# Optimization experiments

Measured on AMD Instinct MI355X. Metric: run time of the kernel, lower is better.

The kernel has to match this reference:

```python
import jax, jax.numpy as jnp
import numpy as np

B, CIN, H = 8192, 512, 2048  # batch, in_channels, hidden_channels


def _ln(x, g, b, eps=1e-5):
    m = jnp.mean(x, axis=-1, keepdims=True)
    v = jnp.var(x, axis=-1, keepdims=True)
    return (x - m) * jax.lax.rsqrt(v + eps) * g + b


def setup_inputs() -> dict:
    key = jax.random.key(0)
    ks = jax.random.split(key, 16)
    d = {
        'x': jax.random.normal(ks[0], (B, 1, CIN), jnp.float32),
        'h': jax.random.normal(ks[1], (B, H), jnp.float32),
        'c': jax.random.normal(ks[2], (B, H), jnp.float32),
        # input_proj: in_channels -> hidden
        'W_proj': jax.random.normal(ks[3], (H, CIN), jnp.float32) / np.sqrt(CIN),
        'b_proj': jnp.zeros((H,), jnp.float32),
        # layerNorm over concat(x_proj, h) of width 2H
        'g_ln': jnp.ones((2 * H,), jnp.float32),
        'b_ln': jnp.zeros((2 * H,), jnp.float32),
        # cell_norm / hidden_norm
        'g_cn': jnp.ones((H,), jnp.float32),
        'b_cn': jnp.zeros((H,), jnp.float32),
        'g_hn': jnp.ones((H,), jnp.float32),
        'b_hn': jnp.zeros((H,), jnp.float32),
    }
    for name, k in zip(['f', 'i', 'c2', 'o'], ks[4:8]):
        d[f'W_{name}'] = jax.random.normal(k, (H, 2 * H), jnp.float32) / np.sqrt(2 * H)
        d[f'b_{name}'] = jnp.zeros((H,), jnp.float32)
        d[f'g_{name}'] = jnp.ones((H,), jnp.float32)
        d[f'beta_{name}'] = jnp.zeros((H,), jnp.float32)
    return d


def reference(x, h, c, W_proj, b_proj, g_ln, b_ln, g_cn, b_cn, g_hn, b_hn,
              W_f, b_f, g_f, beta_f, W_i, b_i, g_i, beta_i,
              W_c2, b_c2, g_c2, beta_c2, W_o, b_o, g_o, beta_o):
    # x: [B,1,CIN] -> squeeze, project to hidden width (CIN != H branch)
    xp = x[:, 0, :] @ W_proj.T + b_proj                      # [B,H]
    combined = jnp.concatenate([xp, h], axis=-1)             # [B,2H]
    combined = jnp.tanh(_ln(combined, g_ln, b_ln))           # activation = tanh
    # four gate blocks: Linear(2H->H) + LayerNorm (dropout = identity in eval)
    f = jax.nn.sigmoid(_ln(combined @ W_f.T + b_f, g_f, beta_f))
    i = jax.nn.sigmoid(_ln(combined @ W_i.T + b_i, g_i, beta_i))
    o = jax.nn.sigmoid(_ln(combined @ W_o.T + b_o, g_o, beta_o))
    cc = jnp.tanh(_ln(combined @ W_c2.T + b_c2, g_c2, beta_c2))
    next_cell = _ln(f * c + i * cc, g_cn, b_cn)
    next_hidden = jnp.tanh(_ln(o * jnp.tanh(next_cell), g_hn, b_hn))
    # original returns (next_hidden, (next_hidden, next_cell)); stack the two states
    return jnp.stack([next_hidden, next_cell])               # [2,B,H]
```

## Files before the change

kernel.cpp:

```cpp
#include <hip/hip_runtime.h>
#include <stdint.h>


#define BM 128
#define BN 128
#define BK 32

typedef __attribute__((ext_vector_type(8))) short short8;
typedef __attribute__((ext_vector_type(4))) float f32x4;

__device__ __forceinline__ unsigned short f2bf(float x) {
  union { float f; uint32_t u; } v; v.f = x;
  uint32_t r = v.u + 0x7FFFu + ((v.u >> 16) & 1u);
  return (unsigned short)(r >> 16);
}
__device__ __forceinline__ float bf2f(unsigned short u) {
  union { uint32_t u; float f; } v; v.u = ((uint32_t)u) << 16; return v.f;
}
__device__ __forceinline__ void unpack8(uint4 p, float* o) {
  uint32_t w[4] = {p.x, p.y, p.z, p.w};
#pragma unroll
  for (int k = 0; k < 4; k++) {
    o[2*k]   = bf2f((unsigned short)(w[k] & 0xffffu));
    o[2*k+1] = bf2f((unsigned short)(w[k] >> 16));
  }
}
__device__ __forceinline__ uint4 pack8(const float* s) {
  uint4 r;
  r.x = (uint32_t)f2bf(s[0]) | ((uint32_t)f2bf(s[1]) << 16);
  r.y = (uint32_t)f2bf(s[2]) | ((uint32_t)f2bf(s[3]) << 16);
  r.z = (uint32_t)f2bf(s[4]) | ((uint32_t)f2bf(s[5]) << 16);
  r.w = (uint32_t)f2bf(s[6]) | ((uint32_t)f2bf(s[7]) << 16);
  return r;
}
__device__ __forceinline__ float tanh_fast(float x) {
  x = fminf(fmaxf(x, -15.f), 15.f);
  float e = __expf(-2.f * x);
  return (1.f - e) / (1.f + e);
}
__device__ __forceinline__ float sigmoid_fast(float x) {
  return 1.f / (1.f + __expf(-x));
}

__global__ __launch_bounds__(256)
void cvt_all(const float* __restrict__ x, const float* __restrict__ Wp,
             const float* __restrict__ Wf, const float* __restrict__ Wi,
             const float* __restrict__ Wc2, const float* __restrict__ Wo,
             unsigned short* __restrict__ xbf, unsigned short* __restrict__ wpbf,
             unsigned short* __restrict__ Wcat) {
  const int blk = blockIdx.x;
  const float* src;
  unsigned short* dst;
  int i;
  if (blk < 2048) {
    src = x; dst = xbf; i = blk * 256 + threadIdx.x;
  } else if (blk < 2560) {
    src = Wp; dst = wpbf; i = (blk - 2048) * 256 + threadIdx.x;
  } else {
    int b2 = blk - 2560;
    int w = b2 >> 12;
    src = (w == 0) ? Wf : (w == 1) ? Wi : (w == 2) ? Wc2 : Wo;
    dst = Wcat + (size_t)w * 8388608;
    i = (b2 & 4095) * 256 + threadIdx.x;
  }
  const float4* s4 = (const float4*)src;
  float4 a = s4[2*i], b = s4[2*i+1];
  float t[8] = {a.x,a.y,a.z,a.w,b.x,b.y,b.z,b.w};
  ((uint4*)dst)[i] = pack8(t);
}

__global__ __launch_bounds__(256, 4)
void gemm_bt_bf16(const unsigned short* __restrict__ A,
                  const unsigned short* __restrict__ Bw,
                  const float* __restrict__ b0, const float* __restrict__ b1,
                  const float* __restrict__ b2, const float* __restrict__ b3,
                  unsigned short* __restrict__ C,
                  int M, int N, int K) {
  __shared__ unsigned short As[BM * BK];
  __shared__ unsigned short Bs[BN * BK];
  const int tid  = threadIdx.x;
  const int lane = tid & 63;
  const int wave = tid >> 6;
  const int wr = wave >> 1, wc = wave & 1;
  const int bm = blockIdx.y * BM;
  const int bn = blockIdx.x * BN;

  const int srow = wave * 16 + (lane >> 2);
  const int schunk = (lane & 3) ^ ((lane >> 2) & 3);
  const int scol = schunk * 8;
  const unsigned short* gA0 = A  + (size_t)(bm + srow)      * K + scol;
  const unsigned short* gA1 = A  + (size_t)(bm + 64 + srow) * K + scol;
  const unsigned short* gB0 = Bw + (size_t)(bn + srow)      * K + scol;
  const unsigned short* gB1 = Bw + (size_t)(bn + 64 + srow) * K + scol;
  unsigned short* lA0 = As + (wave * 16) * BK;
  unsigned short* lA1 = As + (64 + wave * 16) * BK;
  unsigned short* lB0 = Bs + (wave * 16) * BK;
  unsigned short* lB1 = Bs + (64 + wave * 16) * BK;

  const int cl = lane & 15, q = lane >> 4;
  const int sq = q ^ (cl & 3);
  const int a_base = (wr * 64 + cl) * BK + sq * 8;
  const int b_base = (wc * 64 + cl) * BK + sq * 8;

  f32x4 acc[4][4];
#pragma unroll
  for (int i = 0; i < 4; i++)
#pragma unroll
    for (int j = 0; j < 4; j++) acc[i][j] = (f32x4){0.f, 0.f, 0.f, 0.f};

  for (int k0 = 0; k0 < K; k0 += BK) {
    __syncthreads();
    __builtin_amdgcn_global_load_lds(
        (const __attribute__((address_space(1))) void*)(gA0 + k0),
        (__attribute__((address_space(3))) void*)lA0, 16, 0, 0);
    __builtin_amdgcn_global_load_lds(
        (const __attribute__((address_space(1))) void*)(gA1 + k0),
        (__attribute__((address_space(3))) void*)lA1, 16, 0, 0);
    __builtin_amdgcn_global_load_lds(
        (const __attribute__((address_space(1))) void*)(gB0 + k0),
        (__attribute__((address_space(3))) void*)lB0, 16, 0, 0);
    __builtin_amdgcn_global_load_lds(
        (const __attribute__((address_space(1))) void*)(gB1 + k0),
        (__attribute__((address_space(3))) void*)lB1, 16, 0, 0);
    __syncthreads();

    short8 af[4], bv[4];
#pragma unroll
    for (int i = 0; i < 4; i++) af[i] = *(const short8*)(As + a_base + i * 16 * BK);
#pragma unroll
    for (int j = 0; j < 4; j++) bv[j] = *(const short8*)(Bs + b_base + j * 16 * BK);
#pragma unroll
    for (int i = 0; i < 4; i++)
#pragma unroll
      for (int j = 0; j < 4; j++)
        acc[i][j] = __builtin_amdgcn_mfma_f32_16x16x32_bf16(af[i], bv[j], acc[i][j], 0, 0, 0);
  }

#pragma unroll
  for (int i = 0; i < 4; i++) {
    int row0 = bm + wr * 64 + i * 16 + q * 4;
#pragma unroll
    for (int j = 0; j < 4; j++) {
      int col = bn + wc * 64 + j * 16 + cl;
      int gate = col >> 11;
      const float* bp = (gate == 0) ? b0 : (gate == 1) ? b1 : (gate == 2) ? b2 : b3;
      float bvl = bp[col & 2047];
#pragma unroll
      for (int r = 0; r < 4; r++)
        C[(size_t)(row0 + r) * N + col] = f2bf(acc[i][j][r] + bvl);
    }
  }
}

__device__ __forceinline__ float2 block_sum2(float a, float b, float* scr, int t) {
#pragma unroll
  for (int o = 32; o; o >>= 1) { a += __shfl_xor(a, o); b += __shfl_xor(b, o); }
  __syncthreads();
  if ((t & 63) == 0) { scr[(t >> 6) * 2] = a; scr[(t >> 6) * 2 + 1] = b; }
  __syncthreads();
  return make_float2(scr[0] + scr[2] + scr[4] + scr[6],
                     scr[1] + scr[3] + scr[5] + scr[7]);
}

__global__ __launch_bounds__(256)
void ln_tanh_combined(const unsigned short* __restrict__ xp,
                      const float* __restrict__ h,
                      const float* __restrict__ g_ln, const float* __restrict__ b_ln,
                      unsigned short* __restrict__ comb) {
  __shared__ float red[8];
  const int b = blockIdx.x, t = threadIdx.x;
  float xv[8], hv[8];
  unpack8(((const uint4*)(xp + (size_t)b * 2048))[t], xv);
  const float4* hr = (const float4*)(h + (size_t)b * 2048);
  float4 h0 = hr[2*t], h1 = hr[2*t+1];
  hv[0]=h0.x; hv[1]=h0.y; hv[2]=h0.z; hv[3]=h0.w;
  hv[4]=h1.x; hv[5]=h1.y; hv[6]=h1.z; hv[7]=h1.w;
  float s = 0.f, ss = 0.f;
#pragma unroll
  for (int e = 0; e < 8; e++) {
    s += xv[e] + hv[e];
    ss += xv[e]*xv[e] + hv[e]*hv[e];
  }
  float2 r = block_sum2(s, ss, red, t);
  float mean = r.x * (1.f/4096.f);
  float var  = r.y * (1.f/4096.f) - mean*mean;
  float rs = rsqrtf(var + 1e-5f);
  float o0[8], o1[8];
  const int j0 = t * 8;
#pragma unroll
  for (int e = 0; e < 8; e++) {
    int j = j0 + e;
    o0[e] = tanh_fast((xv[e] - mean) * rs * g_ln[j] + b_ln[j]);
  }
#pragma unroll
  for (int e = 0; e < 8; e++) {
    int j = 2048 + j0 + e;
    o1[e] = tanh_fast((hv[e] - mean) * rs * g_ln[j] + b_ln[j]);
  }
  uint4* cr = (uint4*)(comb + (size_t)b * 4096);
  cr[t] = pack8(o0);
  cr[256 + t] = pack8(o1);
}

__global__ __launch_bounds__(256)
void finalize(const unsigned short* __restrict__ gates, const float* __restrict__ c,
              const float* __restrict__ g_f,  const float* __restrict__ bt_f,
              const float* __restrict__ g_i,  const float* __restrict__ bt_i,
              const float* __restrict__ g_c2, const float* __restrict__ bt_c2,
              const float* __restrict__ g_o,  const float* __restrict__ bt_o,
              const float* __restrict__ g_cn, const float* __restrict__ b_cn,
              const float* __restrict__ g_hn, const float* __restrict__ b_hn,
              float* __restrict__ out) {
  __shared__ float red32[32];
  const int b = blockIdx.x, t = threadIdx.x;
  const unsigned short* gr = gates + (size_t)b * 8192;
  float fv[8], iv[8], c2v[8], ov[8];
  unpack8(((const uint4*)(gr        ))[t], fv);
  unpack8(((const uint4*)(gr + 2048))[t], iv);
  unpack8(((const uint4*)(gr + 4096))[t], c2v);
  unpack8(((const uint4*)(gr + 6144))[t], ov);

  float s[8] = {0,0,0,0,0,0,0,0};
#pragma unroll
  for (int e = 0; e < 8; e++) {
    s[0] += fv[e];  s[1] += fv[e]*fv[e];
    s[2] += iv[e];  s[3] += iv[e]*iv[e];
    s[4] += c2v[e]; s[5] += c2v[e]*c2v[e];
    s[6] += ov[e];  s[7] += ov[e]*ov[e];
  }
#pragma unroll
  for (int o = 32; o; o >>= 1)
#pragma unroll
    for (int q2 = 0; q2 < 8; q2++) s[q2] += __shfl_xor(s[q2], o);
  if ((t & 63) == 0) {
#pragma unroll
    for (int q2 = 0; q2 < 8; q2++) red32[(t >> 6) * 8 + q2] = s[q2];
  }
  __syncthreads();
#pragma unroll
  for (int q2 = 0; q2 < 8; q2++)
    s[q2] = red32[q2] + red32[8 + q2] + red32[16 + q2] + red32[24 + q2];

  const float inv = 1.f / 2048.f;
  float m_f = s[0]*inv, rs_f = rsqrtf(s[1]*inv - m_f*m_f + 1e-5f);
  float m_i = s[2]*inv, rs_i = rsqrtf(s[3]*inv - m_i*m_i + 1e-5f);
  float m_c = s[4]*inv, rs_c = rsqrtf(s[5]*inv - m_c*m_c + 1e-5f);
  float m_o = s[6]*inv, rs_o = rsqrtf(s[7]*inv - m_o*m_o + 1e-5f);

  const int j0 = t * 8;
  float cv[8];
  const float4* crp = (const float4*)(c + (size_t)b * 2048);
  float4 c0 = crp[2*t], c1 = crp[2*t+1];
  cv[0]=c0.x; cv[1]=c0.y; cv[2]=c0.z; cv[3]=c0.w;
  cv[4]=c1.x; cv[5]=c1.y; cv[6]=c1.z; cv[7]=c1.w;

  float cellraw[8], os[8];
  float s2 = 0.f, ss2 = 0.f;
#pragma unroll
  for (int e = 0; e < 8; e++) {
    int j = j0 + e;
    float fgate = sigmoid_fast((fv[e]  - m_f) * rs_f * g_f[j]  + bt_f[j]);
    float igate = sigmoid_fast((iv[e]  - m_i) * rs_i * g_i[j]  + bt_i[j]);
    float cgate = tanh_fast   ((c2v[e] - m_c) * rs_c * g_c2[j] + bt_c2[j]);
    os[e]       = sigmoid_fast((ov[e]  - m_o) * rs_o * g_o[j]  + bt_o[j]);
    cellraw[e] = fgate * cv[e] + igate * cgate;
    s2 += cellraw[e]; ss2 += cellraw[e]*cellraw[e];
  }
  float2 rc = block_sum2(s2, ss2, red32, t);
  float m2 = rc.x * inv, rs2 = rsqrtf(rc.y * inv - m2*m2 + 1e-5f);

  float nc[8], hraw[8];
  float s3 = 0.f, ss3 = 0.f;
#pragma unroll
  for (int e = 0; e < 8; e++) {
    int j = j0 + e;
    nc[e] = (cellraw[e] - m2) * rs2 * g_cn[j] + b_cn[j];
    hraw[e] = os[e] * tanh_fast(nc[e]);
    s3 += hraw[e]; ss3 += hraw[e]*hraw[e];
  }
  float2 rh = block_sum2(s3, ss3, red32, t);
  float m3 = rh.x * inv, rs3 = rsqrtf(rh.y * inv - m3*m3 + 1e-5f);

  float nh[8];
#pragma unroll
  for (int e = 0; e < 8; e++) {
    int j = j0 + e;
    nh[e] = tanh_fast((hraw[e] - m3) * rs3 * g_hn[j] + b_hn[j]);
  }
  float4* oh = (float4*)(out + (size_t)b * 2048 + j0);
  oh[0] = make_float4(nh[0], nh[1], nh[2], nh[3]);
  oh[1] = make_float4(nh[4], nh[5], nh[6], nh[7]);
  float4* oc = (float4*)(out + 16777216ull + (size_t)b * 2048 + j0);
  oc[0] = make_float4(nc[0], nc[1], nc[2], nc[3]);
  oc[1] = make_float4(nc[4], nc[5], nc[6], nc[7]);
}

extern "C" void kernel_launch(void* const* d_in, const int* in_sizes, int n_in,
                              void* d_out, int out_size, void* d_ws, size_t ws_size,
                              hipStream_t stream) {
  const float* x      = (const float*)d_in[0];
  const float* h      = (const float*)d_in[1];
  const float* c      = (const float*)d_in[2];
  const float* W_proj = (const float*)d_in[3];
  const float* b_proj = (const float*)d_in[4];
  const float* g_ln   = (const float*)d_in[5];
  const float* b_ln   = (const float*)d_in[6];
  const float* g_cn   = (const float*)d_in[7];
  const float* b_cn   = (const float*)d_in[8];
  const float* g_hn   = (const float*)d_in[9];
  const float* b_hn   = (const float*)d_in[10];
  const float* W_f    = (const float*)d_in[11];
  const float* b_f    = (const float*)d_in[12];
  const float* g_f    = (const float*)d_in[13];
  const float* bt_f   = (const float*)d_in[14];
  const float* W_i    = (const float*)d_in[15];
  const float* b_i    = (const float*)d_in[16];
  const float* g_i    = (const float*)d_in[17];
  const float* bt_i   = (const float*)d_in[18];
  const float* W_c2   = (const float*)d_in[19];
  const float* b_c2   = (const float*)d_in[20];
  const float* g_c2   = (const float*)d_in[21];
  const float* bt_c2  = (const float*)d_in[22];
  const float* W_o    = (const float*)d_in[23];
  const float* b_o    = (const float*)d_in[24];
  const float* g_o    = (const float*)d_in[25];
  const float* bt_o   = (const float*)d_in[26];
  float* out = (float*)d_out;
  char* ws = (char*)d_ws;

  unsigned short* Wcat  = (unsigned short*)(ws);
  unsigned short* comb  = (unsigned short*)(ws + 67108864ull);
  unsigned short* gates = (unsigned short*)(ws + 134217728ull);
  unsigned short* xbf   = (unsigned short*)(ws + 134217728ull);
  unsigned short* wpbf  = (unsigned short*)(ws + 142606336ull);
  unsigned short* xpbf  = (unsigned short*)(ws + 144703488ull);

  cvt_all<<<18944, 256, 0, stream>>>(x, W_proj, W_f, W_i, W_c2, W_o,
                                     xbf, wpbf, Wcat);

  dim3 g1(2048 / BN, 8192 / BM);
  gemm_bt_bf16<<<g1, 256, 0, stream>>>(xbf, wpbf, b_proj, b_proj, b_proj, b_proj,
                                       xpbf, 8192, 2048, 512);

  ln_tanh_combined<<<8192, 256, 0, stream>>>(xpbf, h, g_ln, b_ln, comb);

  dim3 g2(8192 / BN, 8192 / BM);
  gemm_bt_bf16<<<g2, 256, 0, stream>>>(comb, Wcat, b_f, b_i, b_c2, b_o,
                                       gates, 8192, 8192, 4096);

  finalize<<<8192, 256, 0, stream>>>(gates, c, g_f, bt_f, g_i, bt_i, g_c2, bt_c2,
                                     g_o, bt_o, g_cn, b_cn, g_hn, b_hn, out);
}
```

Measured before the change: 1.104 ms.

## Replace GEMM with 256x256 double-buffered 8-phase pipelined MFMA kernel

Replaces the simple 128x128x32 single-buffered bf16 GEMM with a 256x256 tile, 512-thread kernel. It double-buffers 64-wide K slices in LDS and splits each iteration into eight phases that interleave global-to-LDS prefetches with MFMA bursts, using setprio and explicit waitcnt/barriers. It also remaps block IDs across 8 groups (likely XCD-aware) and uses an XOR swizzle for the larger LDS rows. The aim is to raise MFMA utilisation and hide load latency, at the cost of heavy register use (128 accumulator floats per thread), more LDS per block, and fragile hand-written synchronisation.

```diff
diff --git a/kernel.cpp b/kernel.cpp
--- a/kernel.cpp
+++ b/kernel.cpp
@@ -1,10 +1,6 @@
 #include <hip/hip_runtime.h>
 #include <stdint.h>
 
-
-#define BM 128
-#define BN 128
-#define BK 32
 
 typedef __attribute__((ext_vector_type(8))) short short8;
 typedef __attribute__((ext_vector_type(4))) float f32x4;
@@ -69,88 +65,226 @@
   ((uint4*)dst)[i] = pack8(t);
 }
 
-__global__ __launch_bounds__(256, 4)
-void gemm_bt_bf16(const unsigned short* __restrict__ A,
-                  const unsigned short* __restrict__ Bw,
-                  const float* __restrict__ b0, const float* __restrict__ b1,
-                  const float* __restrict__ b2, const float* __restrict__ b3,
-                  unsigned short* __restrict__ C,
-                  int M, int N, int K) {
-  __shared__ unsigned short As[BM * BK];
-  __shared__ unsigned short Bs[BN * BK];
+#define MFMA16(a, b, c) __builtin_amdgcn_mfma_f32_16x16x32_bf16((a), (b), (c), 0, 0, 0)
+#define GLDS16(g, l)                                                         \
+  __builtin_amdgcn_global_load_lds(                                          \
+      (const __attribute__((address_space(1))) void*)(g),                    \
+      (__attribute__((address_space(3))) void*)(l), 16, 0, 0)
+
+__global__ __launch_bounds__(512, 2)
+void gemm_8ph(const unsigned short* __restrict__ A,
+              const unsigned short* __restrict__ Bw,
+              const float* __restrict__ b0, const float* __restrict__ b1,
+              const float* __restrict__ b2, const float* __restrict__ b3,
+              unsigned short* __restrict__ C,
+              int M, int N, int K) {
+  __shared__ __align__(16) unsigned short As[2][2][128][64];
+  __shared__ __align__(16) unsigned short Bs[2][2][128][64];
+
   const int tid  = threadIdx.x;
   const int lane = tid & 63;
-  const int wave = tid >> 6;
-  const int wr = wave >> 1, wc = wave & 1;
-  const int bm = blockIdx.y * BM;
-  const int bn = blockIdx.x * BN;
-
-  const int srow = wave * 16 + (lane >> 2);
-  const int schunk = (lane & 3) ^ ((lane >> 2) & 3);
-  const int scol = schunk * 8;
-  const unsigned short* gA0 = A  + (size_t)(bm + srow)      * K + scol;
-  const unsigned short* gA1 = A  + (size_t)(bm + 64 + srow) * K + scol;
-  const unsigned short* gB0 = Bw + (size_t)(bn + srow)      * K + scol;
-  const unsigned short* gB1 = Bw + (size_t)(bn + 64 + srow) * K + scol;
-  unsigned short* lA0 = As + (wave * 16) * BK;
-  unsigned short* lA1 = As + (64 + wave * 16) * BK;
-  unsigned short* lB0 = Bs + (wave * 16) * BK;
-  unsigned short* lB1 = Bs + (64 + wave * 16) * BK;
+  const int wv   = tid >> 6;
+  const int wm   = wv >> 2;
+  const int wn   = wv & 3;
+
+  const int nbx = N >> 8;
+  const int nwg = (M >> 8) * nbx;
+  const int bid = blockIdx.x;
+  const int cpx = nwg >> 3;
+  const int tile = (nwg & 7) ? bid : (bid & 7) * cpx + (bid >> 3);
+  const int bm = (tile / nbx) << 8;
+  const int bn = (tile % nbx) << 8;
+
+  const int srow = wv * 8 + (lane >> 3);
+  const int schk = (lane & 7) ^ (lane >> 3);
+  const unsigned short* ag = A  + (size_t)(bm + srow) * K + schk * 8;
+  const unsigned short* bg = Bw + (size_t)(bn + srow) * K + schk * 8;
+
+#define STAGE_A(t, h)                                                        \
+  do {                                                                       \
+    GLDS16(ag + (size_t)((h) * 128)      * K + (t) * 64,                     \
+           &As[(t) & 1][(h)][wv * 8][0]);                                    \
+    GLDS16(ag + (size_t)((h) * 128 + 64) * K + (t) * 64,                     \
+           &As[(t) & 1][(h)][64 + wv * 8][0]);                               \
+  } while (0)
+#define STAGE_B(t, h)                                                        \
+  do {                                                                       \
+    GLDS16(bg + (size_t)((h) * 128)      * K + (t) * 64,                     \
+           &Bs[(t) & 1][(h)][wv * 8][0]);                                    \
+    GLDS16(bg + (size_t)((h) * 128 + 64) * K + (t) * 64,                     \
+           &Bs[(t) & 1][(h)][64 + wv * 8][0]);                               \
+  } while (0)
 
   const int cl = lane & 15, q = lane >> 4;
-  const int sq = q ^ (cl & 3);
-  const int a_base = (wr * 64 + cl) * BK + sq * 8;
-  const int b_base = (wc * 64 + cl) * BK + sq * 8;
-
-  f32x4 acc[4][4];
-#pragma unroll
-  for (int i = 0; i < 4; i++)
-#pragma unroll
-    for (int j = 0; j < 4; j++) acc[i][j] = (f32x4){0.f, 0.f, 0.f, 0.f};
-
-  for (int k0 = 0; k0 < K; k0 += BK) {
-    __syncthreads();
-    __builtin_amdgcn_global_load_lds(
-        (const __attribute__((address_space(1))) void*)(gA0 + k0),
-        (__attribute__((address_space(3))) void*)lA0, 16, 0, 0);
-    __builtin_amdgcn_global_load_lds(
-        (const __attribute__((address_space(1))) void*)(gA1 + k0),
-        (__attribute__((address_space(3))) void*)lA1, 16, 0, 0);
-    __builtin_amdgcn_global_load_lds(
-        (const __attribute__((address_space(1))) void*)(gB0 + k0),
-        (__attribute__((address_space(3))) void*)lB0, 16, 0, 0);
-    __builtin_amdgcn_global_load_lds(
-        (const __attribute__((address_space(1))) void*)(gB1 + k0),
-        (__attribute__((address_space(3))) void*)lB1, 16, 0, 0);
-    __syncthreads();
-
-    short8 af[4], bv[4];
-#pragma unroll
-    for (int i = 0; i < 4; i++) af[i] = *(const short8*)(As + a_base + i * 16 * BK);
-#pragma unroll
-    for (int j = 0; j < 4; j++) bv[j] = *(const short8*)(Bs + b_base + j * 16 * BK);
-#pragma unroll
-    for (int i = 0; i < 4; i++)
-#pragma unroll
-      for (int j = 0; j < 4; j++)
-        acc[i][j] = __builtin_amdgcn_mfma_f32_16x16x32_bf16(af[i], bv[j], acc[i][j], 0, 0, 0);
-  }
-
-#pragma unroll
-  for (int i = 0; i < 4; i++) {
-    int row0 = bm + wr * 64 + i * 16 + q * 4;
-#pragma unroll
-    for (int j = 0; j < 4; j++) {
-      int col = bn + wc * 64 + j * 16 + cl;
-      int gate = col >> 11;
+  const int ard0 = cl * 64 + ((q       ^ (cl & 7)) * 8);
+  const int ard1 = cl * 64 + (((4 | q) ^ (cl & 7)) * 8);
+  const int brd0 = ((wn & 1) * 64 + cl) * 64 + ((q       ^ (cl & 7)) * 8);
+  const int brd1 = ((wn & 1) * 64 + cl) * 64 + (((4 | q) ^ (cl & 7)) * 8);
+  const unsigned short* pa0 = &As[0][wm][0][0];
+  const unsigned short* pa1 = &As[1][wm][0][0];
+  const unsigned short* pb0 = &Bs[0][wn >> 1][0][0];
+  const unsigned short* pb1 = &Bs[1][wn >> 1][0][0];
+
+  STAGE_A(0, 0); STAGE_A(0, 1); STAGE_B(0, 0); STAGE_B(0, 1);
+  STAGE_A(1, 0);
+
+  f32x4 acc[8][4];
+#pragma unroll
+  for (int r = 0; r < 8; ++r)
+#pragma unroll
+    for (int j = 0; j < 4; ++j) acc[r][j] = (f32x4){0.f, 0.f, 0.f, 0.f};
+
+  asm volatile("s_waitcnt vmcnt(2)");
+  __builtin_amdgcn_s_barrier();
+
+  short8 af[8], bv[4];
+  const int NI = K >> 7;
+
+  for (int i = 0; i < NI; ++i) {
+    const int t = 2 * i;
+    const bool pf = (i + 1 < NI);
+
+#pragma unroll
+    for (int r = 0; r < 8; ++r) af[r] = *(const short8*)(pa0 + ard0 + r * 1024);
+    bv[0] = *(const short8*)(pb0 + brd0);
+    bv[1] = *(const short8*)(pb0 + brd0 + 1024);
+    STAGE_A(t + 1, 1);
+    __builtin_amdgcn_s_barrier();
+    asm volatile("s_waitcnt lgkmcnt(0)");
+    __builtin_amdgcn_s_setprio(1);
+#pragma unroll
+    for (int r = 0; r < 8; ++r) {
+      acc[r][0] = MFMA16(af[r], bv[0], acc[r][0]);
+      acc[r][1] = MFMA16(af[r], bv[1], acc[r][1]);
+    }
+    __builtin_amdgcn_s_setprio(0);
+    __builtin_amdgcn_s_barrier();
+
+    bv[2] = *(const short8*)(pb0 + brd0 + 2048);
+    bv[3] = *(const short8*)(pb0 + brd0 + 3072);
+    STAGE_B(t + 1, 0);
+    __builtin_amdgcn_s_barrier();
+    asm volatile("s_waitcnt lgkmcnt(0)");
+    __builtin_amdgcn_s_setprio(1);
+#pragma unroll
+    for (int r = 0; r < 8; ++r) {
+      acc[r][2] = MFMA16(af[r], bv[2], acc[r][2]);
+      acc[r][3] = MFMA16(af[r], bv[3], acc[r][3]);
+    }
+    __builtin_amdgcn_s_setprio(0);
+    __builtin_amdgcn_s_barrier();
+
+#pragma unroll
+    for (int r = 0; r < 8; ++r) af[r] = *(const short8*)(pa0 + ard1 + r * 1024);
+    bv[0] = *(const short8*)(pb0 + brd1);
+    bv[1] = *(const short8*)(pb0 + brd1 + 1024);
+    STAGE_B(t + 1, 1);
+    __builtin_amdgcn_s_barrier();
+    asm volatile("s_waitcnt lgkmcnt(0)");
+    __builtin_amdgcn_s_setprio(1);
+#pragma unroll
+    for (int r = 0; r < 8; ++r) {
+      acc[r][0] = MFMA16(af[r], bv[0], acc[r][0]);
+      acc[r][1] = MFMA16(af[r], bv[1], acc[r][1]);
+    }
+    __builtin_amdgcn_s_setprio(0);
+    __builtin_amdgcn_s_barrier();
+
+    bv[2] = *(const short8*)(pb0 + brd1 + 2048);
+    bv[3] = *(const short8*)(pb0 + brd1 + 3072);
+    if (pf) STAGE_A(t + 2, 0);
+    __builtin_amdgcn_s_barrier();
+    asm volatile("s_waitcnt lgkmcnt(0)");
+    __builtin_amdgcn_s_setprio(1);
+#pragma unroll
+    for (int r = 0; r < 8; ++r) {
+      acc[r][2] = MFMA16(af[r], bv[2], acc[r][2]);
+      acc[r][3] = MFMA16(af[r], bv[3], acc[r][3]);
+    }
+    __builtin_amdgcn_s_setprio(0);
+    if (pf) { asm volatile("s_waitcnt vmcnt(2)"); }
+    else    { asm volatile("s_waitcnt vmcnt(0)"); }
+    __builtin_amdgcn_s_barrier();
+
+#pragma unroll
+    for (int r = 0; r < 8; ++r) af[r] = *(const short8*)(pa1 + ard0 + r * 1024);
+    bv[0] = *(const short8*)(pb1 + brd0);
+    bv[1] = *(const short8*)(pb1 + brd0 + 1024);
+    if (pf) STAGE_A(t + 2, 1);
+    __builtin_amdgcn_s_barrier();
+    asm volatile("s_waitcnt lgkmcnt(0)");
+    __builtin_amdgcn_s_setprio(1);
+#pragma unroll
+    for (int r = 0; r < 8; ++r) {
+      acc[r][0] = MFMA16(af[r], bv[0], acc[r][0]);
+      acc[r][1] = MFMA16(af[r], bv[1], acc[r][1]);
+    }
+    __builtin_amdgcn_s_setprio(0);
+    __builtin_amdgcn_s_barrier();
+
+    bv[2] = *(const short8*)(pb1 + brd0 + 2048);
+    bv[3] = *(const short8*)(pb1 + brd0 + 3072);
+    if (pf) STAGE_B(t + 2, 0);
+    __builtin_amdgcn_s_barrier();
+    asm volatile("s_waitcnt lgkmcnt(0)");
+    __builtin_amdgcn_s_setprio(1);
+#pragma unroll
+    for (int r = 0; r < 8; ++r) {
+      acc[r][2] = MFMA16(af[r], bv[2], acc[r][2]);
+      acc[r][3] = MFMA16(af[r], bv[3], acc[r][3]);
+    }
+    __builtin_amdgcn_s_setprio(0);
+    __builtin_amdgcn_s_barrier();
+
+#pragma unroll
+    for (int r = 0; r < 8; ++r) af[r] = *(const short8*)(pa1 + ard1 + r * 1024);
+    bv[0] = *(const short8*)(pb1 + brd1);
+    bv[1] = *(const short8*)(pb1 + brd1 + 1024);
+    if (pf) STAGE_B(t + 2, 1);
+    __builtin_amdgcn_s_barrier();
+    asm volatile("s_waitcnt lgkmcnt(0)");
+    __builtin_amdgcn_s_setprio(1);
+#pragma unroll
+    for (int r = 0; r < 8; ++r) {
+      acc[r][0] = MFMA16(af[r], bv[0], acc[r][0]);
+      acc[r][1] = MFMA16(af[r], bv[1], acc[r][1]);
+    }
+    __builtin_amdgcn_s_setprio(0);
+    __builtin_amdgcn_s_barrier();
+
+    bv[2] = *(const short8*)(pb1 + brd1 + 2048);
+    bv[3] = *(const short8*)(pb1 + brd1 + 3072);
+    if (pf) STAGE_A(t + 3, 0);
+    __builtin_amdgcn_s_barrier();
+    asm volatile("s_waitcnt lgkmcnt(0)");
+    __builtin_amdgcn_s_setprio(1);
+#pragma unroll
+    for (int r = 0; r < 8; ++r) {
+      acc[r][2] = MFMA16(af[r], bv[2], acc[r][2]);
+      acc[r][3] = MFMA16(af[r], bv[3], acc[r][3]);
+    }
+    __builtin_amdgcn_s_setprio(0);
+    if (pf) { asm volatile("s_waitcnt vmcnt(2)"); }
+    __builtin_amdgcn_s_barrier();
+  }
+
+#pragma unroll
+  for (int r8 = 0; r8 < 8; ++r8) {
+    const int row0 = bm + wm * 128 + r8 * 16 + q * 4;
+#pragma unroll
+    for (int j = 0; j < 4; ++j) {
+      const int col = bn + wn * 64 + j * 16 + cl;
+      const int gate = col >> 11;
       const float* bp = (gate == 0) ? b0 : (gate == 1) ? b1 : (gate == 2) ? b2 : b3;
-      float bvl = bp[col & 2047];
-#pragma unroll
-      for (int r = 0; r < 4; r++)
-        C[(size_t)(row0 + r) * N + col] = f2bf(acc[i][j][r] + bvl);
-    }
-  }
-}
+      const float bb = bp[col & 2047];
+#pragma unroll
+      for (int rr = 0; rr < 4; ++rr)
+        C[(size_t)(row0 + rr) * N + col] = f2bf(acc[r8][j][rr] + bb);
+    }
+  }
+}
+#undef STAGE_A
+#undef STAGE_B
 
 __device__ __forceinline__ float2 block_sum2(float a, float b, float* scr, int t) {
 #pragma unroll
@@ -338,15 +472,13 @@
   cvt_all<<<18944, 256, 0, stream>>>(x, W_proj, W_f, W_i, W_c2, W_o,
                                      xbf, wpbf, Wcat);
 
-  dim3 g1(2048 / BN, 8192 / BM);
-  gemm_bt_bf16<<<g1, 256, 0, stream>>>(xbf, wpbf, b_proj, b_proj, b_proj, b_proj,
-                                       xpbf, 8192, 2048, 512);
+  gemm_8ph<<<dim3(256), dim3(512), 0, stream>>>(
+      xbf, wpbf, b_proj, b_proj, b_proj, b_proj, xpbf, 8192, 2048, 512);
 
   ln_tanh_combined<<<8192, 256, 0, stream>>>(xpbf, h, g_ln, b_ln, comb);
 
-  dim3 g2(8192 / BN, 8192 / BM);
-  gemm_bt_bf16<<<g2, 256, 0, stream>>>(comb, Wcat, b_f, b_i, b_c2, b_o,
-                                       gates, 8192, 8192, 4096);
+  gemm_8ph<<<dim3(1024), dim3(512), 0, stream>>>(
+      comb, Wcat, b_f, b_i, b_c2, b_o, gates, 8192, 8192, 4096);
 
   finalize<<<8192, 256, 0, stream>>>(gates, c, g_f, bt_f, g_i, bt_i, g_c2, bt_c2,
                                      g_o, bt_o, g_cn, b_cn, g_hn, b_hn, out);
```

Result: faster. 1.036 ms (-6.2%).
